# Kernel optimization log

Measured on AMD Instinct MI355X. Metric: run time of the kernel, lower is better.

Reference implementation:

```python
import jax, jax.numpy as jnp
import numpy as np

N_NODES = 100000
NEG_SLOPE = 0.2  # PyG GATConv default


def setup_inputs() -> dict:
    key = jax.random.key(0)
    ks = jax.random.split(key, 12)
    F, H1, H2, C, E = 128, 128, 16, 2, 600000
    s = lambda k, shape, fan: jax.random.normal(k, shape, jnp.float32) * (1.0 / np.sqrt(fan))
    return {
        "x": jax.random.normal(ks[0], (N_NODES, F), jnp.float32),
        "edge_index": jax.random.randint(ks[1], (2, E), 0, N_NODES, jnp.int64),
        "W": s(ks[2], (F, F), F),
        "a_src": s(ks[3], (F,), F),
        "a_dst": s(ks[4], (F,), F),
        "bias_gat": jnp.zeros((F,), jnp.float32),
        "W1": s(ks[5], (2 * F, H1), 2 * F),
        "b1": jnp.zeros((H1,), jnp.float32),
        "W2": s(ks[6], (H1, H2), H1),
        "b2": jnp.zeros((H2,), jnp.float32),
        "W3": s(ks[7], (H2, C), H2),
        "b3": jnp.zeros((C,), jnp.float32),
    }


def _gat_conv(x, edge_index, W, a_src, a_dst, bias_gat):
    N = x.shape[0]
    # add self loops (PyG default)
    loops = jnp.arange(N, dtype=edge_index.dtype)
    src = jnp.concatenate([edge_index[0], loops])
    dst = jnp.concatenate([edge_index[1], loops])
    xp = x @ W                                   # [N, F] transformed features
    alpha_s = xp @ a_src                         # [N]
    alpha_d = xp @ a_dst                         # [N]
    e = alpha_s[src] + alpha_d[dst]              # [E+N]
    e = jnp.where(e >= 0, e, NEG_SLOPE * e)      # leaky relu
    # segment softmax over incoming edges of each destination node
    e_max = jax.ops.segment_max(e, dst, num_segments=N)
    e_exp = jnp.exp(e - e_max[dst])
    denom = jax.ops.segment_sum(e_exp, dst, num_segments=N)
    alpha = e_exp / denom[dst]                   # [E+N]
    out = jax.ops.segment_sum(alpha[:, None] * xp[src], dst, num_segments=N)
    return out + bias_gat


def reference(x, edge_index, W, a_src, a_dst, bias_gat, W1, b1, W2, b2, W3, b3):
    x_embedded = _gat_conv(x, edge_index, W, a_src, a_dst, bias_gat)
    x_e = jax.nn.relu(x_embedded)                # dropout is identity in eval
    h = jnp.concatenate([x, x_e], axis=1)        # [N, 2F]
    h = jax.nn.relu(h @ W1 + b1)
    h = jax.nn.relu(h @ W2 + b2)
    logits = h @ W3 + b3
    return (x_embedded, jax.nn.sigmoid(logits))
```

## Files before the change

### kernel.cpp

```cpp
#include <hip/hip_runtime.h>

#define F 128
#define LEAK 0.2f

typedef __attribute__((ext_vector_type(8))) short bf16x8;
typedef __attribute__((ext_vector_type(4))) float f32x4;

union FragU { bf16x8 v; unsigned u[4]; };

__device__ inline unsigned f2bf(float f) {
  unsigned u = __float_as_uint(f);
  return (u + 0x7FFFu + ((u >> 16) & 1u)) >> 16;
}
__device__ inline unsigned packbf(float lo, float hi) {
  return f2bf(lo) | (f2bf(hi) << 16);
}
__device__ inline float bflo(unsigned u) { return __uint_as_float(u << 16); }
__device__ inline float bfhi(unsigned u) { return __uint_as_float(u & 0xFFFF0000u); }

__device__ inline void edge_sd(const int* ei, int i, int E, int is64, int& s, int& d) {
  if (i < E) {
    if (is64) {
      const long long* e64 = (const long long*)ei;
      s = (int)e64[i]; d = (int)e64[E + i];
    } else {
      s = ei[i]; d = ei[E + i];
    }
  } else {
    s = d = i - E;
  }
}

__global__ void zero_detect_kernel(const int* ei, int* flag, int* deg,
                                   int* cursor, int N) {
  int i = blockIdx.x * blockDim.x + threadIdx.x;
  if (i < N) { deg[i] = 0; cursor[i] = 0; }
  if (blockIdx.x == 0) {
    __shared__ int any;
    if (threadIdx.x == 0) any = 0;
    __syncthreads();
    for (int k = threadIdx.x; k < 1024; k += blockDim.x)
      if (ei[2 * k + 1] != 0) any = 1;
    __syncthreads();
    if (threadIdx.x == 0) *flag = (any == 0) ? 1 : 0;
  }
}

__global__ void count_kernel(const int* ei, int* deg, const int* flag, int E, int N) {
  int i = blockIdx.x * blockDim.x + threadIdx.x;
  if (i >= E + N) return;
  int s, d;
  edge_sd(ei, i, E, *flag, s, d);
  atomicAdd(&deg[d], 1);
}

__global__ void scan1_kernel(const int* deg, int* partial, int N) {
  __shared__ int ts[256];
  int b = blockIdx.x, t = threadIdx.x;
  int base = b * 1024 + t * 4;
  int s = 0;
#pragma unroll
  for (int k = 0; k < 4; ++k) s += (base + k < N) ? deg[base + k] : 0;
  ts[t] = s;
  __syncthreads();
  for (int o = 128; o > 0; o >>= 1) {
    if (t < o) ts[t] += ts[t + o];
    __syncthreads();
  }
  if (t == 0) partial[b] = ts[0];
}

__global__ void scan2_kernel(const int* partial, int* chunk_off, int* row_start,
                             int nchunks, int N) {
  __shared__ int ts[256];
  int t = threadIdx.x;
  int v = (t < nchunks) ? partial[t] : 0;
  ts[t] = v;
  __syncthreads();
  for (int o = 1; o < 256; o <<= 1) {
    int add = (t >= o) ? ts[t - o] : 0;
    __syncthreads();
    ts[t] += add;
    __syncthreads();
  }
  if (t < nchunks) chunk_off[t] = ts[t] - v;
  if (t == nchunks - 1) row_start[N] = ts[t];
}

__global__ void scan3_kernel(const int* deg, const int* chunk_off,
                             int* row_start, int N) {
  __shared__ int ts[256];
  int b = blockIdx.x, t = threadIdx.x;
  int base = b * 1024 + t * 4;
  int v[4];
#pragma unroll
  for (int k = 0; k < 4; ++k) v[k] = (base + k < N) ? deg[base + k] : 0;
  int p1 = v[0], p2 = p1 + v[1], p3 = p2 + v[2], sum = p3 + v[3];
  ts[t] = sum;
  __syncthreads();
  for (int o = 1; o < 256; o <<= 1) {
    int add = (t >= o) ? ts[t - o] : 0;
    __syncthreads();
    ts[t] += add;
    __syncthreads();
  }
  int off = chunk_off[b] + ts[t] - sum;
  int ex[4] = {0, p1, p2, p3};
#pragma unroll
  for (int k = 0; k < 4; ++k)
    if (base + k < N) row_start[base + k] = off + ex[k];
}

__global__ void fill_kernel(const int* ei, const int* row_start, int* cursor,
                            int* sorted_src, const int* flag, int E, int N) {
  int i = blockIdx.x * blockDim.x + threadIdx.x;
  if (i >= E + N) return;
  int s, d;
  edge_sd(ei, i, E, *flag, s, d);
  int p = atomicAdd(&cursor[d], 1);
  sorted_src[row_start[d] + p] = s;
}

__global__ void prep_kernel(const float* __restrict__ W,
                            const float* __restrict__ W1, unsigned* wt,
                            unsigned* w1t) {
  int i = blockIdx.x * 256 + threadIdx.x;
  if (i < 128 * 64) {
    int n = i & 127, k2 = i >> 7;
    wt[n * 64 + k2] =
        packbf(W[(size_t)(2 * k2) * 128 + n], W[(size_t)(2 * k2 + 1) * 128 + n]);
  }
  int j = i - 128 * 64;
  if (j >= 0 && j < 128 * 128) {
    int n = j & 127, k2 = j >> 7;
    w1t[n * 128 + k2] = packbf(W1[(size_t)(2 * k2) * 128 + n],
                               W1[(size_t)(2 * k2 + 1) * 128 + n]);
  }
}

__global__ __launch_bounds__(512) void gemm_xp_kernel(
    const float* __restrict__ x, const unsigned* __restrict__ wt,
    const float* __restrict__ a_src, const float* __restrict__ a_dst,
    unsigned short* __restrict__ xp, float* __restrict__ alpha_s,
    float* __restrict__ alpha_d, int N, int ntiles) {
  __shared__ char WtL[128 * 256];
  __shared__ char stage[8 * 4096];
  const int tid = threadIdx.x;
  const int w = tid >> 6, l = tid & 63;
  const int lr = l & 15, lg = l >> 4;
  char* st = stage + w * 4096;

  for (int c = tid; c < 2048; c += 512) {
    int n = c >> 4, q = c & 15;
    uint4 v = *(const uint4*)(wt + n * 64 + q * 4);
    *(uint4*)(WtL + n * 256 + ((q * 16) ^ ((n & 7) << 4))) = v;
  }

  float asv[8], adv[8];
#pragma unroll
  for (int f = 0; f < 8; ++f) {
    asv[f] = a_src[f * 16 + lr];
    adv[f] = a_dst[f * 16 + lr];
  }
  __syncthreads();

  for (int t = blockIdx.x; t < ntiles; t += gridDim.x) {
    const int rbase = t * 128 + w * 16;
    const int rc = min(rbase + lr, N - 1);
    const float* xrow = x + (size_t)rc * 128;

    FragU a[4];
#pragma unroll
    for (int ks = 0; ks < 4; ++ks) {
      float4 p0 = *(const float4*)(xrow + ks * 32 + lg * 8);
      float4 p1 = *(const float4*)(xrow + ks * 32 + lg * 8 + 4);
      a[ks].u[0] = packbf(p0.x, p0.y); a[ks].u[1] = packbf(p0.z, p0.w);
      a[ks].u[2] = packbf(p1.x, p1.y); a[ks].u[3] = packbf(p1.z, p1.w);
    }

    f32x4 acc[8];
#pragma unroll
    for (int f = 0; f < 8; ++f) acc[f] = (f32x4){0.f, 0.f, 0.f, 0.f};

#pragma unroll
    for (int ks = 0; ks < 4; ++ks) {
#pragma unroll
      for (int f = 0; f < 8; ++f) {
        int n = f * 16 + lr;
        FragU bfr;
        bfr.v = *(const bf16x8*)(WtL + n * 256 +
                                 ((ks * 64 + lg * 16) ^ ((n & 7) << 4)));
        acc[f] = __builtin_amdgcn_mfma_f32_16x16x32_bf16(a[ks].v, bfr.v,
                                                         acc[f], 0, 0, 0);
      }
    }

#pragma unroll
    for (int r = 0; r < 4; ++r) {
      int orow = rbase + lg * 4 + r;
      float ps = 0.f, pd = 0.f;
#pragma unroll
      for (int f = 0; f < 8; ++f) {
        ps = fmaf(acc[f][r], asv[f], ps);
        pd = fmaf(acc[f][r], adv[f], pd);
      }
#pragma unroll
      for (int m = 1; m < 16; m <<= 1) {
        ps += __shfl_xor(ps, m);
        pd += __shfl_xor(pd, m);
      }
      if (orow < N && lr == 0) alpha_s[orow] = ps;
      if (orow < N && lr == 1) alpha_d[orow] = pd;
    }

#pragma unroll
    for (int f = 0; f < 8; ++f) {
      int colb = (f * 16 + lr) * 2;
#pragma unroll
      for (int r = 0; r < 4; ++r) {
        int row = lg * 4 + r;
        *(unsigned short*)(st + row * 256 + (colb ^ ((row & 7) << 4))) =
            (unsigned short)f2bf(acc[f][r]);
      }
    }
#pragma unroll
    for (int it = 0; it < 4; ++it) {
      int off = it * 1024 + l * 16;
      int row = off >> 8, colb = off & 255;
      int4 v = *(const int4*)(st + row * 256 + (colb ^ ((row & 7) << 4)));
      int grow = rbase + row;
      if (grow < N) *(int4*)((char*)xp + (size_t)grow * 256 + colb) = v;
    }
  }
}

__global__ __launch_bounds__(256) void gather_kernel(
    const int* __restrict__ row_start, const int* __restrict__ sorted_src,
    const float* __restrict__ alpha_s, const float* __restrict__ alpha_d,
    const unsigned short* __restrict__ xp, const float* __restrict__ bias,
    float* __restrict__ out0, int N) {
  int wid = blockIdx.x * 4 + (threadIdx.x >> 6);
  int lane = threadIdx.x & 63;
  if (wid >= N) return;
  int rs = row_start[wid], re = row_start[wid + 1];
  int deg = re - rs;
  float ad = alpha_d[wid];

  if (deg <= 64) {
    const int half = lane >> 5;
    const int hl = lane & 31;

    int src_reg = 0;
    float e = -INFINITY;
    if (lane < deg) {
      src_reg = sorted_src[rs + lane];
      e = alpha_s[src_reg] + ad;
      e = (e >= 0.f) ? e : LEAK * e;
    }
    float m = e;
#pragma unroll
    for (int o = 32; o > 0; o >>= 1) m = fmaxf(m, __shfl_xor(m, o));
    float ex = (lane < deg) ? expf(e - m) : 0.f;
    float lsum = ex;
#pragma unroll
    for (int o = 32; o > 0; o >>= 1) lsum += __shfl_xor(lsum, o);
    float w_reg = ex / lsum;

    float c0 = 0.f, c1 = 0.f, c2 = 0.f, c3 = 0.f;
    int j = 0;
    for (; j + 3 < deg; j += 4) {
      int jj0 = j + half, jj1 = j + 2 + half;
      int s0 = __shfl(src_reg, jj0), s1 = __shfl(src_reg, jj1);
      float w0 = __shfl(w_reg, jj0), w1 = __shfl(w_reg, jj1);
      uint2 u0 = *(const uint2*)(xp + (size_t)s0 * 128 + hl * 4);
      uint2 u1 = *(const uint2*)(xp + (size_t)s1 * 128 + hl * 4);
      c0 = fmaf(w0, bflo(u0.x), c0); c1 = fmaf(w0, bfhi(u0.x), c1);
      c2 = fmaf(w0, bflo(u0.y), c2); c3 = fmaf(w0, bfhi(u0.y), c3);
      c0 = fmaf(w1, bflo(u1.x), c0); c1 = fmaf(w1, bfhi(u1.x), c1);
      c2 = fmaf(w1, bflo(u1.y), c2); c3 = fmaf(w1, bfhi(u1.y), c3);
    }
    for (; j < deg; j += 2) {
      int jj = j + half;
      int s0 = __shfl(src_reg, jj);
      float w0 = __shfl(w_reg, jj);
      uint2 u0 = *(const uint2*)(xp + (size_t)s0 * 128 + hl * 4);
      c0 = fmaf(w0, bflo(u0.x), c0); c1 = fmaf(w0, bfhi(u0.x), c1);
      c2 = fmaf(w0, bflo(u0.y), c2); c3 = fmaf(w0, bfhi(u0.y), c3);
    }
    c0 += __shfl_xor(c0, 32); c1 += __shfl_xor(c1, 32);
    c2 += __shfl_xor(c2, 32); c3 += __shfl_xor(c3, 32);
    if (half == 0) {
      float4 bv = *(const float4*)(bias + hl * 4);
      *(float4*)(out0 + (size_t)wid * F + hl * 4) =
          make_float4(c0 + bv.x, c1 + bv.y, c2 + bv.z, c3 + bv.w);
    }
  } else {
    float a0 = 0.f, a1 = 0.f;
    float m = -INFINITY;
    for (int j = lane; j < deg; j += 64) {
      float e = alpha_s[sorted_src[rs + j]] + ad;
      e = (e >= 0.f) ? e : LEAK * e;
      m = fmaxf(m, e);
    }
#pragma unroll
    for (int o = 32; o > 0; o >>= 1) m = fmaxf(m, __shfl_xor(m, o));
    float lsum = 0.f;
    for (int j = lane; j < deg; j += 64) {
      float e = alpha_s[sorted_src[rs + j]] + ad;
      e = (e >= 0.f) ? e : LEAK * e;
      lsum += expf(e - m);
    }
#pragma unroll
    for (int o = 32; o > 0; o >>= 1) lsum += __shfl_xor(lsum, o);
    float inv = 1.f / lsum;
    for (int j = 0; j < deg; ++j) {
      int s0 = sorted_src[rs + j];
      float e = alpha_s[s0] + ad;
      e = (e >= 0.f) ? e : LEAK * e;
      float w0 = expf(e - m) * inv;
      unsigned u0 = *(const unsigned*)(xp + (size_t)s0 * 128 + lane * 2);
      a0 = fmaf(w0, bflo(u0), a0); a1 = fmaf(w0, bfhi(u0), a1);
    }
    float2 bv = *(const float2*)(bias + lane * 2);
    *(float2*)(out0 + (size_t)wid * F + lane * 2) =
        make_float2(a0 + bv.x, a1 + bv.y);
  }
}

__global__ __launch_bounds__(512) void mlp_kernel(
    const float* __restrict__ x, const float* __restrict__ xemb,
    const unsigned* __restrict__ w1t, const float* __restrict__ b1,
    const float* __restrict__ W2, const float* __restrict__ b2,
    const float* __restrict__ W3, const float* __restrict__ b3,
    float* __restrict__ out2, int N, int ntiles) {
  __shared__ char W1L[128 * 256];
  __shared__ char W2t[16 * 256];
  __shared__ char h1s[128 * 256];
  const int tid = threadIdx.x;

  for (int idx = tid; idx < 16 * 64; idx += 512) {
    int n = idx & 15, k = (idx >> 4) * 2;
    unsigned p = packbf(W2[(size_t)k * 16 + n], W2[(size_t)(k + 1) * 16 + n]);
    *(unsigned*)(W2t + n * 256 + ((k * 2) ^ ((n & 7) << 4))) = p;
  }

  const int w = tid >> 6, l = tid & 63;
  const int lr = l & 15, lg = l >> 4;
  float b1v[8];
#pragma unroll
  for (int f = 0; f < 8; ++f) b1v[f] = b1[f * 16 + lr];
  const float b2v = b2[lr];
  const float w30 = W3[lr * 2 + 0], w31 = W3[lr * 2 + 1];
  const float b30 = b3[0], b31 = b3[1];

  for (int t = blockIdx.x; t < ntiles; t += gridDim.x) {
    const int rbase = t * 128 + w * 16;
    const int rc = min(rbase + lr, N - 1);
    const float* xrow = x + (size_t)rc * 128;
    const float* erow = xemb + (size_t)rc * 128;

    f32x4 acc[8];
#pragma unroll
    for (int f = 0; f < 8; ++f) acc[f] = (f32x4){0.f, 0.f, 0.f, 0.f};

#pragma unroll
    for (int hh = 0; hh < 2; ++hh) {
      __syncthreads();
      for (int c = tid; c < 2048; c += 512) {
        int n = c >> 4, q = c & 15;
        uint4 v = *(const uint4*)(w1t + n * 128 + hh * 64 + q * 4);
        *(uint4*)(W1L + n * 256 + ((q * 16) ^ ((n & 7) << 4))) = v;
      }
      __syncthreads();

      FragU a[4];
#pragma unroll
      for (int ks = 0; ks < 4; ++ks) {
        const float* src = (hh == 0) ? (xrow + ks * 32 + lg * 8)
                                     : (erow + ks * 32 + lg * 8);
        float4 p0 = *(const float4*)(src);
        float4 p1 = *(const float4*)(src + 4);
        if (hh == 1) {
          p0.x = fmaxf(p0.x, 0.f); p0.y = fmaxf(p0.y, 0.f);
          p0.z = fmaxf(p0.z, 0.f); p0.w = fmaxf(p0.w, 0.f);
          p1.x = fmaxf(p1.x, 0.f); p1.y = fmaxf(p1.y, 0.f);
          p1.z = fmaxf(p1.z, 0.f); p1.w = fmaxf(p1.w, 0.f);
        }
        a[ks].u[0] = packbf(p0.x, p0.y); a[ks].u[1] = packbf(p0.z, p0.w);
        a[ks].u[2] = packbf(p1.x, p1.y); a[ks].u[3] = packbf(p1.z, p1.w);
      }

#pragma unroll
      for (int ks = 0; ks < 4; ++ks) {
#pragma unroll
        for (int f = 0; f < 8; ++f) {
          int n = f * 16 + lr;
          FragU bfr;
          bfr.v = *(const bf16x8*)(W1L + n * 256 +
                                   ((ks * 64 + lg * 16) ^ ((n & 7) << 4)));
          acc[f] = __builtin_amdgcn_mfma_f32_16x16x32_bf16(a[ks].v, bfr.v,
                                                           acc[f], 0, 0, 0);
        }
      }
    }

#pragma unroll
    for (int f = 0; f < 8; ++f) {
      int col = f * 16 + lr;
#pragma unroll
      for (int r = 0; r < 4; ++r) {
        int hrow = w * 16 + lg * 4 + r;
        float v = fmaxf(acc[f][r] + b1v[f], 0.f);
        *(unsigned short*)(h1s + hrow * 256 + ((col * 2) ^ ((hrow & 7) << 4))) =
            (unsigned short)f2bf(v);
      }
    }

    f32x4 acc2 = (f32x4){0.f, 0.f, 0.f, 0.f};
#pragma unroll
    for (int ks = 0; ks < 4; ++ks) {
      int hrow = w * 16 + lr;
      FragU af, bfr;
      af.v = *(const bf16x8*)(h1s + hrow * 256 +
                              ((ks * 64 + lg * 16) ^ ((hrow & 7) << 4)));
      bfr.v = *(const bf16x8*)(W2t + lr * 256 +
                               ((ks * 64 + lg * 16) ^ ((lr & 7) << 4)));
      acc2 = __builtin_amdgcn_mfma_f32_16x16x32_bf16(af.v, bfr.v, acc2, 0, 0, 0);
    }

#pragma unroll
    for (int r = 0; r < 4; ++r) {
      float h2 = fmaxf(acc2[r] + b2v, 0.f);
      float t0 = h2 * w30, t1 = h2 * w31;
#pragma unroll
      for (int m = 1; m < 16; m <<= 1) {
        t0 += __shfl_xor(t0, m);
        t1 += __shfl_xor(t1, m);
      }
      int orow = rbase + lg * 4 + r;
      if (orow < N && lr < 2) {
        float s = (lr == 0) ? (t0 + b30) : (t1 + b31);
        out2[(size_t)orow * 2 + lr] = 1.f / (1.f + expf(-s));
      }
    }
  }
}

extern "C" void kernel_launch(void* const* d_in, const int* in_sizes, int n_in,
                              void* d_out, int out_size, void* d_ws,
                              size_t ws_size, hipStream_t stream) {
  const float* x     = (const float*)d_in[0];
  const int*   ei    = (const int*)d_in[1];
  const float* W     = (const float*)d_in[2];
  const float* a_src = (const float*)d_in[3];
  const float* a_dst = (const float*)d_in[4];
  const float* bias  = (const float*)d_in[5];
  const float* W1    = (const float*)d_in[6];
  const float* b1    = (const float*)d_in[7];
  const float* W2    = (const float*)d_in[8];
  const float* b2    = (const float*)d_in[9];
  const float* W3    = (const float*)d_in[10];
  const float* b3    = (const float*)d_in[11];

  const int N = in_sizes[0] / F;
  const int E = in_sizes[1] / 2;
  const int EN = E + N;
  const int nchunks = (N + 1023) / 1024;
  const int ntiles = (N + 127) / 128;

  float* ws = (float*)d_ws;
  unsigned short* xp = (unsigned short*)ws;
  float* alpha_s  = ws + (size_t)N * 64;
  float* alpha_d  = alpha_s + N;
  unsigned* wt    = (unsigned*)(alpha_d + N);
  unsigned* w1t   = wt + 128 * 64;
  int* deg        = (int*)(w1t + 128 * 128);
  int* row_start  = deg + N;
  int* cursor     = row_start + N + 1;
  int* partial    = cursor + N;
  int* chunk_off  = partial + 256;
  int* sorted_src = chunk_off + 256;
  int* flag       = sorted_src + EN;

  float* out0 = (float*)d_out;
  float* out2 = out0 + (size_t)N * F;

  zero_detect_kernel<<<(N + 255) / 256, 256, 0, stream>>>(ei, flag, deg,
                                                          cursor, N);
  count_kernel<<<(EN + 255) / 256, 256, 0, stream>>>(ei, deg, flag, E, N);
  scan1_kernel<<<nchunks, 256, 0, stream>>>(deg, partial, N);
  scan2_kernel<<<1, 256, 0, stream>>>(partial, chunk_off, row_start, nchunks, N);
  scan3_kernel<<<nchunks, 256, 0, stream>>>(deg, chunk_off, row_start, N);
  fill_kernel<<<(EN + 255) / 256, 256, 0, stream>>>(ei, row_start, cursor,
                                                    sorted_src, flag, E, N);
  prep_kernel<<<96, 256, 0, stream>>>(W, W1, wt, w1t);
  gemm_xp_kernel<<<512, 512, 0, stream>>>(x, wt, a_src, a_dst, xp, alpha_s,
                                          alpha_d, N, ntiles);
  gather_kernel<<<(N + 3) / 4, 256, 0, stream>>>(row_start, sorted_src, alpha_s,
                                                 alpha_d, xp, bias, out0, N);
  mlp_kernel<<<512, 512, 0, stream>>>(x, out0, w1t, b1, W2, b2, W3, b3, out2, N,
                                      ntiles);
}
```

Measured before the change: 178.1 us.

## Merge setup kernels, write bf16 relu embedding for MLP, shrink LDS for occupancy

Folds weight prep into the init kernel and scan2 into scan3, which removes two launches. The gather kernel now also writes a bf16 copy of relu(x_embedded), so the MLP reads half the bytes for its second input. LDS use drops in gemm_xp (staging in two phases) and in mlp (W1 staged in four quarters), and both grids grow to 768 blocks to raise occupancy. In exchange, every scan3 block recomputes the chunk prefix, the MLP adds more syncthreads rounds, and an extra N×128 bf16 workspace is written.

```diff
diff --git a/kernel.cpp b/kernel.cpp
--- a/kernel.cpp
+++ b/kernel.cpp
@@ -31,18 +31,35 @@
   }
 }
 
-__global__ void zero_detect_kernel(const int* ei, int* flag, int* deg,
-                                   int* cursor, int N) {
-  int i = blockIdx.x * blockDim.x + threadIdx.x;
-  if (i < N) { deg[i] = 0; cursor[i] = 0; }
-  if (blockIdx.x == 0) {
-    __shared__ int any;
-    if (threadIdx.x == 0) any = 0;
-    __syncthreads();
-    for (int k = threadIdx.x; k < 1024; k += blockDim.x)
-      if (ei[2 * k + 1] != 0) any = 1;
-    __syncthreads();
-    if (threadIdx.x == 0) *flag = (any == 0) ? 1 : 0;
+__global__ void init_kernel(const int* ei, int* flag, int* deg, int* cursor,
+                            const float* __restrict__ W,
+                            const float* __restrict__ W1, unsigned* wt,
+                            unsigned* w1t, int N, int nzb) {
+  if ((int)blockIdx.x < nzb) {
+    int i = blockIdx.x * blockDim.x + threadIdx.x;
+    if (i < N) { deg[i] = 0; cursor[i] = 0; }
+    if (blockIdx.x == 0) {
+      __shared__ int any;
+      if (threadIdx.x == 0) any = 0;
+      __syncthreads();
+      for (int k = threadIdx.x; k < 1024; k += blockDim.x)
+        if (ei[2 * k + 1] != 0) any = 1;
+      __syncthreads();
+      if (threadIdx.x == 0) *flag = (any == 0) ? 1 : 0;
+    }
+    return;
+  }
+  int i = (blockIdx.x - nzb) * 256 + threadIdx.x;
+  if (i < 128 * 64) {
+    int n = i & 127, k2 = i >> 7;
+    wt[n * 64 + k2] =
+        packbf(W[(size_t)(2 * k2) * 128 + n], W[(size_t)(2 * k2 + 1) * 128 + n]);
+  }
+  int j = i - 128 * 64;
+  if (j >= 0 && j < 128 * 128) {
+    int n = j & 127, k2 = j >> 7;
+    w1t[n * 128 + k2] = packbf(W1[(size_t)(2 * k2) * 128 + n],
+                               W1[(size_t)(2 * k2 + 1) * 128 + n]);
   }
 }
 
@@ -70,27 +87,24 @@
   if (t == 0) partial[b] = ts[0];
 }
 
-__global__ void scan2_kernel(const int* partial, int* chunk_off, int* row_start,
-                             int nchunks, int N) {
+__global__ void scan3_kernel(const int* deg, const int* partial,
+                             int* row_start, int nchunks, int N) {
   __shared__ int ts[256];
-  int t = threadIdx.x;
-  int v = (t < nchunks) ? partial[t] : 0;
-  ts[t] = v;
+  __shared__ int cs[256];
+  int b = blockIdx.x, t = threadIdx.x;
+
+  int pv = (t < nchunks) ? partial[t] : 0;
+  cs[t] = pv;
   __syncthreads();
   for (int o = 1; o < 256; o <<= 1) {
-    int add = (t >= o) ? ts[t - o] : 0;
+    int add = (t >= o) ? cs[t - o] : 0;
     __syncthreads();
-    ts[t] += add;
+    cs[t] += add;
     __syncthreads();
   }
-  if (t < nchunks) chunk_off[t] = ts[t] - v;
-  if (t == nchunks - 1) row_start[N] = ts[t];
-}
-
-__global__ void scan3_kernel(const int* deg, const int* chunk_off,
-                             int* row_start, int N) {
-  __shared__ int ts[256];
-  int b = blockIdx.x, t = threadIdx.x;
+  if (b == 0 && t == 0) row_start[N] = cs[nchunks - 1];
+  int chunk_off_b = cs[b] - partial[b];
+
   int base = b * 1024 + t * 4;
   int v[4];
 #pragma unroll
@@ -104,7 +118,7 @@
     ts[t] += add;
     __syncthreads();
   }
-  int off = chunk_off[b] + ts[t] - sum;
+  int off = chunk_off_b + ts[t] - sum;
   int ex[4] = {0, p1, p2, p3};
 #pragma unroll
   for (int k = 0; k < 4; ++k)
@@ -121,34 +135,17 @@
   sorted_src[row_start[d] + p] = s;
 }
 
-__global__ void prep_kernel(const float* __restrict__ W,
-                            const float* __restrict__ W1, unsigned* wt,
-                            unsigned* w1t) {
-  int i = blockIdx.x * 256 + threadIdx.x;
-  if (i < 128 * 64) {
-    int n = i & 127, k2 = i >> 7;
-    wt[n * 64 + k2] =
-        packbf(W[(size_t)(2 * k2) * 128 + n], W[(size_t)(2 * k2 + 1) * 128 + n]);
-  }
-  int j = i - 128 * 64;
-  if (j >= 0 && j < 128 * 128) {
-    int n = j & 127, k2 = j >> 7;
-    w1t[n * 128 + k2] = packbf(W1[(size_t)(2 * k2) * 128 + n],
-                               W1[(size_t)(2 * k2 + 1) * 128 + n]);
-  }
-}
-
 __global__ __launch_bounds__(512) void gemm_xp_kernel(
     const float* __restrict__ x, const unsigned* __restrict__ wt,
     const float* __restrict__ a_src, const float* __restrict__ a_dst,
     unsigned short* __restrict__ xp, float* __restrict__ alpha_s,
     float* __restrict__ alpha_d, int N, int ntiles) {
   __shared__ char WtL[128 * 256];
-  __shared__ char stage[8 * 4096];
+  __shared__ char stage[8 * 2048];
   const int tid = threadIdx.x;
   const int w = tid >> 6, l = tid & 63;
   const int lr = l & 15, lg = l >> 4;
-  char* st = stage + w * 4096;
+  char* st = stage + w * 2048;
 
   for (int c = tid; c < 2048; c += 512) {
     int n = c >> 4, q = c & 15;
@@ -214,22 +211,27 @@
     }
 
 #pragma unroll
-    for (int f = 0; f < 8; ++f) {
-      int colb = (f * 16 + lr) * 2;
-#pragma unroll
-      for (int r = 0; r < 4; ++r) {
-        int row = lg * 4 + r;
-        *(unsigned short*)(st + row * 256 + (colb ^ ((row & 7) << 4))) =
-            (unsigned short)f2bf(acc[f][r]);
-      }
-    }
-#pragma unroll
-    for (int it = 0; it < 4; ++it) {
-      int off = it * 1024 + l * 16;
-      int row = off >> 8, colb = off & 255;
-      int4 v = *(const int4*)(st + row * 256 + (colb ^ ((row & 7) << 4)));
-      int grow = rbase + row;
-      if (grow < N) *(int4*)((char*)xp + (size_t)grow * 256 + colb) = v;
+    for (int ph = 0; ph < 2; ++ph) {
+      if ((lg >> 1) == ph) {
+#pragma unroll
+        for (int f = 0; f < 8; ++f) {
+          int colb = (f * 16 + lr) * 2;
+#pragma unroll
+          for (int r = 0; r < 4; ++r) {
+            int row = (lg & 1) * 4 + r;
+            *(unsigned short*)(st + row * 256 + (colb ^ ((row & 7) << 4))) =
+                (unsigned short)f2bf(acc[f][r]);
+          }
+        }
+      }
+#pragma unroll
+      for (int it = 0; it < 2; ++it) {
+        int off = it * 1024 + l * 16;
+        int row = off >> 8, colb = off & 255;
+        int4 v = *(const int4*)(st + row * 256 + (colb ^ ((row & 7) << 4)));
+        int grow = rbase + ph * 8 + row;
+        if (grow < N) *(int4*)((char*)xp + (size_t)grow * 256 + colb) = v;
+      }
     }
   }
 }
@@ -238,7 +240,7 @@
     const int* __restrict__ row_start, const int* __restrict__ sorted_src,
     const float* __restrict__ alpha_s, const float* __restrict__ alpha_d,
     const unsigned short* __restrict__ xp, const float* __restrict__ bias,
-    float* __restrict__ out0, int N) {
+    float* __restrict__ out0, unsigned short* __restrict__ xe16, int N) {
   int wid = blockIdx.x * 4 + (threadIdx.x >> 6);
   int lane = threadIdx.x & 63;
   if (wid >= N) return;
@@ -289,10 +291,14 @@
     }
     c0 += __shfl_xor(c0, 32); c1 += __shfl_xor(c1, 32);
     c2 += __shfl_xor(c2, 32); c3 += __shfl_xor(c3, 32);
+    float4 bv = *(const float4*)(bias + hl * 4);
+    c0 += bv.x; c1 += bv.y; c2 += bv.z; c3 += bv.w;
     if (half == 0) {
-      float4 bv = *(const float4*)(bias + hl * 4);
-      *(float4*)(out0 + (size_t)wid * F + hl * 4) =
-          make_float4(c0 + bv.x, c1 + bv.y, c2 + bv.z, c3 + bv.w);
+      *(float4*)(out0 + (size_t)wid * F + hl * 4) = make_float4(c0, c1, c2, c3);
+    } else {
+      unsigned lo = packbf(fmaxf(c0, 0.f), fmaxf(c1, 0.f));
+      unsigned hi = packbf(fmaxf(c2, 0.f), fmaxf(c3, 0.f));
+      *(uint2*)(xe16 + (size_t)wid * 128 + hl * 4) = make_uint2(lo, hi);
     }
   } else {
     float a0 = 0.f, a1 = 0.f;
@@ -322,18 +328,20 @@
       a0 = fmaf(w0, bflo(u0), a0); a1 = fmaf(w0, bfhi(u0), a1);
     }
     float2 bv = *(const float2*)(bias + lane * 2);
-    *(float2*)(out0 + (size_t)wid * F + lane * 2) =
-        make_float2(a0 + bv.x, a1 + bv.y);
+    a0 += bv.x; a1 += bv.y;
+    *(float2*)(out0 + (size_t)wid * F + lane * 2) = make_float2(a0, a1);
+    *(unsigned*)(xe16 + (size_t)wid * 128 + lane * 2) =
+        packbf(fmaxf(a0, 0.f), fmaxf(a1, 0.f));
   }
 }
 
 __global__ __launch_bounds__(512) void mlp_kernel(
-    const float* __restrict__ x, const float* __restrict__ xemb,
+    const float* __restrict__ x, const unsigned short* __restrict__ xe16,
     const unsigned* __restrict__ w1t, const float* __restrict__ b1,
     const float* __restrict__ W2, const float* __restrict__ b2,
     const float* __restrict__ W3, const float* __restrict__ b3,
     float* __restrict__ out2, int N, int ntiles) {
-  __shared__ char W1L[128 * 256];
+  __shared__ char W1L[128 * 128];
   __shared__ char W2t[16 * 256];
   __shared__ char h1s[128 * 256];
   const int tid = threadIdx.x;
@@ -357,46 +365,43 @@
     const int rbase = t * 128 + w * 16;
     const int rc = min(rbase + lr, N - 1);
     const float* xrow = x + (size_t)rc * 128;
-    const float* erow = xemb + (size_t)rc * 128;
+    const unsigned short* erow = xe16 + (size_t)rc * 128;
 
     f32x4 acc[8];
 #pragma unroll
     for (int f = 0; f < 8; ++f) acc[f] = (f32x4){0.f, 0.f, 0.f, 0.f};
 
 #pragma unroll
-    for (int hh = 0; hh < 2; ++hh) {
+    for (int q = 0; q < 4; ++q) {
       __syncthreads();
-      for (int c = tid; c < 2048; c += 512) {
-        int n = c >> 4, q = c & 15;
-        uint4 v = *(const uint4*)(w1t + n * 128 + hh * 64 + q * 4);
-        *(uint4*)(W1L + n * 256 + ((q * 16) ^ ((n & 7) << 4))) = v;
+      for (int c = tid; c < 1024; c += 512) {
+        int n = c >> 3, j = (c & 7) * 4;
+        uint4 v = *(const uint4*)(w1t + n * 128 + q * 32 + j);
+        *(uint4*)(W1L + n * 128 + ((j * 4) ^ ((n & 7) << 4))) = v;
       }
       __syncthreads();
 
-      FragU a[4];
-#pragma unroll
-      for (int ks = 0; ks < 4; ++ks) {
-        const float* src = (hh == 0) ? (xrow + ks * 32 + lg * 8)
-                                     : (erow + ks * 32 + lg * 8);
-        float4 p0 = *(const float4*)(src);
-        float4 p1 = *(const float4*)(src + 4);
-        if (hh == 1) {
-          p0.x = fmaxf(p0.x, 0.f); p0.y = fmaxf(p0.y, 0.f);
-          p0.z = fmaxf(p0.z, 0.f); p0.w = fmaxf(p0.w, 0.f);
-          p1.x = fmaxf(p1.x, 0.f); p1.y = fmaxf(p1.y, 0.f);
-          p1.z = fmaxf(p1.z, 0.f); p1.w = fmaxf(p1.w, 0.f);
+      FragU a[2];
+#pragma unroll
+      for (int ks = 0; ks < 2; ++ks) {
+        if (q < 2) {
+          const float* src = xrow + q * 64 + ks * 32 + lg * 8;
+          float4 p0 = *(const float4*)(src);
+          float4 p1 = *(const float4*)(src + 4);
+          a[ks].u[0] = packbf(p0.x, p0.y); a[ks].u[1] = packbf(p0.z, p0.w);
+          a[ks].u[2] = packbf(p1.x, p1.y); a[ks].u[3] = packbf(p1.z, p1.w);
+        } else {
+          a[ks].v = *(const bf16x8*)(erow + (q - 2) * 64 + ks * 32 + lg * 8);
         }
-        a[ks].u[0] = packbf(p0.x, p0.y); a[ks].u[1] = packbf(p0.z, p0.w);
-        a[ks].u[2] = packbf(p1.x, p1.y); a[ks].u[3] = packbf(p1.z, p1.w);
-      }
-
-#pragma unroll
-      for (int ks = 0; ks < 4; ++ks) {
+      }
+
+#pragma unroll
+      for (int ks = 0; ks < 2; ++ks) {
 #pragma unroll
         for (int f = 0; f < 8; ++f) {
           int n = f * 16 + lr;
           FragU bfr;
-          bfr.v = *(const bf16x8*)(W1L + n * 256 +
+          bfr.v = *(const bf16x8*)(W1L + n * 128 +
                                    ((ks * 64 + lg * 16) ^ ((n & 7) << 4)));
           acc[f] = __builtin_amdgcn_mfma_f32_16x16x32_bf16(a[ks].v, bfr.v,
                                                            acc[f], 0, 0, 0);
@@ -467,10 +472,12 @@
   const int EN = E + N;
   const int nchunks = (N + 1023) / 1024;
   const int ntiles = (N + 127) / 128;
+  const int nzb = (N + 255) / 256;
 
   float* ws = (float*)d_ws;
-  unsigned short* xp = (unsigned short*)ws;
-  float* alpha_s  = ws + (size_t)N * 64;
+  unsigned short* xp   = (unsigned short*)ws;
+  unsigned short* xe16 = xp + (size_t)N * 128;
+  float* alpha_s  = ws + (size_t)N * 128;
   float* alpha_d  = alpha_s + N;
   unsigned* wt    = (unsigned*)(alpha_d + N);
   unsigned* w1t   = wt + 128 * 64;
@@ -478,26 +485,24 @@
   int* row_start  = deg + N;
   int* cursor     = row_start + N + 1;
   int* partial    = cursor + N;
-  int* chunk_off  = partial + 256;
-  int* sorted_src = chunk_off + 256;
+  int* sorted_src = partial + 256;
   int* flag       = sorted_src + EN;
 
   float* out0 = (float*)d_out;
   float* out2 = out0 + (size_t)N * F;
 
-  zero_detect_kernel<<<(N + 255) / 256, 256, 0, stream>>>(ei, flag, deg,
-                                                          cursor, N);
+  init_kernel<<<nzb + 96, 256, 0, stream>>>(ei, flag, deg, cursor, W, W1, wt,
+                                            w1t, N, nzb);
   count_kernel<<<(EN + 255) / 256, 256, 0, stream>>>(ei, deg, flag, E, N);
   scan1_kernel<<<nchunks, 256, 0, stream>>>(deg, partial, N);
-  scan2_kernel<<<1, 256, 0, stream>>>(partial, chunk_off, row_start, nchunks, N);
-  scan3_kernel<<<nchunks, 256, 0, stream>>>(deg, chunk_off, row_start, N);
+  scan3_kernel<<<nchunks, 256, 0, stream>>>(deg, partial, row_start, nchunks, N);
   fill_kernel<<<(EN + 255) / 256, 256, 0, stream>>>(ei, row_start, cursor,
                                                     sorted_src, flag, E, N);
-  prep_kernel<<<96, 256, 0, stream>>>(W, W1, wt, w1t);
-  gemm_xp_kernel<<<512, 512, 0, stream>>>(x, wt, a_src, a_dst, xp, alpha_s,
+  gemm_xp_kernel<<<768, 512, 0, stream>>>(x, wt, a_src, a_dst, xp, alpha_s,
                                           alpha_d, N, ntiles);
   gather_kernel<<<(N + 3) / 4, 256, 0, stream>>>(row_start, sorted_src, alpha_s,
-                                                 alpha_d, xp, bias, out0, N);
-  mlp_kernel<<<512, 512, 0, stream>>>(x, out0, w1t, b1, W2, b2, W3, b3, out2, N,
+                                                 alpha_d, xp, bias, out0, xe16,
+                                                 N);
+  mlp_kernel<<<768, 512, 0, stream>>>(x, xe16, w1t, b1, W2, b2, W3, b3, out2, N,
                                       ntiles);
 }
```

Measured after the change: 225.3 us. 26.5% more time.
